# Optimization experiments

Hardware: AMD Instinct MI355X
Metric: run time of the kernel (lower is better)

Reference implementation:

```python
import jax, jax.numpy as jnp
import numpy as np

LAMBDA_DEPTHG = 0.3
STEGO_TEMPERATURE = 0.1
KNN_K = 7
DEPTH_SIGMA = 0.5
EPS = 1e-8


def _l2norm(x):
    return x / jnp.sqrt(jnp.sum(x * x, axis=-1, keepdims=True) + EPS)


def _stego_loss(codes, feats, temperature, knn_k):
    # Pairwise cosine similarity of DINO features -> KNN graph (includes self).
    f = _l2norm(feats)                                  # (B,N,Df)
    sim_f = jnp.einsum('bnd,bmd->bnm', f, f)            # (B,N,N)
    _, knn_idx = jax.lax.top_k(sim_f, knn_k)            # (B,N,k) int32
    # Temperature-scaled InfoNCE over code similarities; KNN entries are positives.
    c = _l2norm(codes)                                  # (B,N,Dc)
    logits = jnp.einsum('bnd,bmd->bnm', c, c) / temperature  # (B,N,N)
    logp = jax.nn.log_softmax(logits, axis=-1)          # (B,N,N)
    pos_logp = jnp.take_along_axis(logp, knn_idx, axis=-1)   # (B,N,k)
    return -jnp.mean(pos_logp)


def _depth_guided_correlation_loss(codes, depth, sigma_d):
    # Gaussian depth affinity: pixels at similar depth should have similar codes.
    dd = depth[:, :, None] - depth[:, None, :]          # (B,N,N)
    w = jnp.exp(-(dd * dd) / (2.0 * sigma_d * sigma_d)) # (B,N,N)
    c = _l2norm(codes)
    s = jnp.einsum('bnd,bmd->bnm', c, c)                # (B,N,N) cosine corr
    return jnp.mean(w * (1.0 - s))


def setup_inputs() -> dict:
    key = jax.random.key(0)
    k1, k2, k3 = jax.random.split(key, 3)
    B, N = 2, 4096
    semantic_codes = jax.random.normal(k1, (B, N, 90), dtype=jnp.float32)
    dino_features = jax.random.normal(k2, (B, N, 384), dtype=jnp.float32)
    depth = jax.random.uniform(k3, (B, N), dtype=jnp.float32)
    return {"semantic_codes": semantic_codes, "dino_features": dino_features, "depth": depth}


def reference(semantic_codes, dino_features, depth):
    l_stego = _stego_loss(semantic_codes, dino_features, STEGO_TEMPERATURE, KNN_K)
    l_depthg = _depth_guided_correlation_loss(semantic_codes, depth, DEPTH_SIGMA)
    total = l_stego + LAMBDA_DEPTHG * l_depthg
    return (l_stego, l_depthg, total)
```

## Files before the change

### kernel.cpp

```cpp
#include <hip/hip_runtime.h>
#include <math.h>

#define NPTS 4096

typedef __attribute__((ext_vector_type(8))) short bf16x8;
typedef __attribute__((ext_vector_type(16))) float f32x16;
typedef long fp8x8;

#define KEEP(x) asm volatile("" : "+v"(x))

__device__ __forceinline__ f32x16 zero16() {
  f32x16 z;
#pragma unroll
  for (int i = 0; i < 16; ++i) z[i] = 0.f;
  return z;
}

__device__ __forceinline__ unsigned packkey(float x, int m) {
  unsigned u = __float_as_uint(x);
  unsigned key = u ^ ((unsigned)((int)u >> 31) | 0x80000000u);
  return (key & 0xFFFFF000u) | (unsigned)m;
}

__device__ __forceinline__ void cas7(unsigned v, unsigned* s) {
#pragma unroll
  for (int t = 0; t < 7; ++t) {
    const unsigned hi = s[t] >= v ? s[t] : v;
    const unsigned lo = s[t] >= v ? v : s[t];
    s[t] = hi;
    v = lo;
  }
}

#define KSENT 0u

__device__ __forceinline__ unsigned bf16pack(float a, float b) {
  unsigned ua = __float_as_uint(a); ua = (ua + 0x7FFFu + ((ua >> 16) & 1u)) >> 16;
  unsigned ub = __float_as_uint(b); ub = (ub + 0x7FFFu + ((ub >> 16) & 1u)) >> 16;
  return ua | (ub << 16);
}

__global__ __launch_bounds__(64) void norm_all(const float* __restrict__ feats,
                                               const float* __restrict__ codes,
                                               unsigned char* __restrict__ Fsw8,
                                               unsigned short* __restrict__ Csw,
                                               float* __restrict__ invc) {
  const int row = blockIdx.x;
  const int lane = threadIdx.x;
  const int b = row >> 12, mt = (row >> 5) & 127, rl = row & 31;

  const float* f = feats + (size_t)row * 384;
  float v[8];
  float ss = 0.f;
  if (lane < 48) {
    float4 p0 = *(const float4*)(f + lane * 8);
    float4 p1 = *(const float4*)(f + lane * 8 + 4);
    v[0] = p0.x; v[1] = p0.y; v[2] = p0.z; v[3] = p0.w;
    v[4] = p1.x; v[5] = p1.y; v[6] = p1.z; v[7] = p1.w;
#pragma unroll
    for (int e = 0; e < 8; ++e) ss = fmaf(v[e], v[e], ss);
  }
#pragma unroll
  for (int m = 1; m <= 32; m <<= 1) ss += __shfl_xor(ss, m, 64);
  const float s8 = rsqrtf(ss + 1e-8f) * 8.0f;
  if (lane < 48) {
    int w0 = __builtin_amdgcn_cvt_pk_fp8_f32(v[0] * s8, v[1] * s8, 0, 0);
    w0 = __builtin_amdgcn_cvt_pk_fp8_f32(v[2] * s8, v[3] * s8, w0, 1);
    int w1 = __builtin_amdgcn_cvt_pk_fp8_f32(v[4] * s8, v[5] * s8, 0, 0);
    w1 = __builtin_amdgcn_cvt_pk_fp8_f32(v[6] * s8, v[7] * s8, w1, 1);
    const int kc = lane >> 1, hs = lane & 1;
    uint2 o = make_uint2((unsigned)w0, (unsigned)w1);
    *(uint2*)(Fsw8 + (((size_t)(b * 128 + mt) * 24 + kc) << 9) + (hs * 32 + rl) * 8) = o;
  }

  const float* c = codes + (size_t)row * 90;
  float cv[8];
#pragma unroll
  for (int e = 0; e < 8; ++e) cv[e] = 0.f;
  if (lane < 11) {
    float4 p0 = *(const float4*)(c + lane * 8);
    float4 p1 = *(const float4*)(c + lane * 8 + 4);
    cv[0] = p0.x; cv[1] = p0.y; cv[2] = p0.z; cv[3] = p0.w;
    cv[4] = p1.x; cv[5] = p1.y; cv[6] = p1.z; cv[7] = p1.w;
  } else if (lane == 11) {
    cv[0] = c[88]; cv[1] = c[89];
  }
  float cs = 0.f;
#pragma unroll
  for (int e = 0; e < 8; ++e) cs = fmaf(cv[e], cv[e], cs);
#pragma unroll
  for (int m = 1; m <= 32; m <<= 1) cs += __shfl_xor(cs, m, 64);
  const float cinv = rsqrtf(cs + 1e-8f);
  if (lane < 12) {
    uint4 o;
    o.x = bf16pack(cv[0] * cinv, cv[1] * cinv);
    o.y = bf16pack(cv[2] * cinv, cv[3] * cinv);
    o.z = bf16pack(cv[4] * cinv, cv[5] * cinv);
    o.w = bf16pack(cv[6] * cinv, cv[7] * cinv);
    const int kc = lane >> 1, hs = lane & 1;
    *(uint4*)(Csw + (((size_t)(b * 128 + mt) * 6 + kc) << 9) + (hs * 32 + rl) * 8) = o;
  }
  if (lane == 0) invc[row] = cinv;
}

__global__ __launch_bounds__(1024) void knn_mfma(const unsigned char* __restrict__ Fsw8,
                                                 unsigned* __restrict__ cand) {
  __shared__ unsigned long long qfrag[2 * 24 * 64];
  __shared__ unsigned ckey[16][64][7];
  const int g = blockIdx.x;
  const int b = g & 1;
  const int h = (g >> 1) & 1;
  const int qp = g >> 2;
  const int q0 = qp * 64;
  const int tid = threadIdx.x;
  const int w = tid >> 6;
  const int lane = tid & 63;
  const int lo = lane & 31, hi4 = (lane >> 5) * 4;
  const unsigned char* Fb = Fsw8 + (size_t)b * 128 * 24 * 512;

  {
    const unsigned long long* src =
        (const unsigned long long*)(Fb + ((size_t)(qp * 2) * 24) * 512);
#pragma unroll
    for (int k = 0; k < 3; ++k) qfrag[tid + k * 1024] = src[tid + k * 1024];
  }
  __syncthreads();

  unsigned s7a[7], s7b[7];
#pragma unroll
  for (int t = 0; t < 7; ++t) { s7a[t] = KSENT; s7b[t] = KSENT; }

  const int t0 = h * 64 + w * 4;
  const unsigned char* ab = Fb + ((size_t)t0 * 24) * 512 + lane * 8;

  fp8x8 a0[12], a1[12], bq[12];
#pragma unroll
  for (int t = 0; t < 12; ++t) a0[t] = *(const fp8x8*)(ab + t * 512);

  for (int mt = 0; mt < 4; ++mt) {
    const unsigned char* art = ab + (size_t)mt * 24 * 512;
#pragma unroll
    for (int t = 0; t < 12; ++t) a1[t] = *(const fp8x8*)(art + (12 + t) * 512);
    f32x16 acc0 = zero16(), acc1 = zero16();
#pragma unroll
    for (int t = 0; t < 12; ++t) bq[t] = (fp8x8)qfrag[t * 64 + lane];
#pragma unroll
    for (int t = 0; t < 12; ++t)
      acc0 = __builtin_amdgcn_mfma_f32_32x32x16_fp8_fp8(a0[t], bq[t], acc0, 0, 0, 0);
#pragma unroll
    for (int t = 0; t < 12; ++t) bq[t] = (fp8x8)qfrag[1536 + t * 64 + lane];
#pragma unroll
    for (int t = 0; t < 12; ++t)
      acc1 = __builtin_amdgcn_mfma_f32_32x32x16_fp8_fp8(a0[t], bq[t], acc1, 0, 0, 0);
#pragma unroll
    for (int t = 0; t < 12; ++t) KEEP(a1[t]);
    if (mt + 1 < 4) {
      const unsigned char* arn = ab + (size_t)(mt + 1) * 24 * 512;
#pragma unroll
      for (int t = 0; t < 12; ++t) a0[t] = *(const fp8x8*)(arn + t * 512);
    }
#pragma unroll
    for (int t = 0; t < 12; ++t) bq[t] = (fp8x8)qfrag[(12 + t) * 64 + lane];
#pragma unroll
    for (int t = 0; t < 12; ++t)
      acc0 = __builtin_amdgcn_mfma_f32_32x32x16_fp8_fp8(a1[t], bq[t], acc0, 0, 0, 0);
#pragma unroll
    for (int t = 0; t < 12; ++t) bq[t] = (fp8x8)qfrag[1536 + (12 + t) * 64 + lane];
#pragma unroll
    for (int t = 0; t < 12; ++t)
      acc1 = __builtin_amdgcn_mfma_f32_32x32x16_fp8_fp8(a1[t], bq[t], acc1, 0, 0, 0);
    const int mb = (t0 + mt) * 32 + hi4;
#pragma unroll
    for (int r = 0; r < 16; ++r) {
      const int m = mb + (r & 3) + 8 * (r >> 2);
      cas7(packkey(acc0[r], m), s7a);
      cas7(packkey(acc1[r], m), s7b);
    }
  }

#pragma unroll
  for (int t = 0; t < 7; ++t) {
    const unsigned ova = (unsigned)__shfl_xor((int)s7a[t], 32, 64);
    const unsigned ovb = (unsigned)__shfl_xor((int)s7b[t], 32, 64);
    cas7(ova, s7a);
    cas7(ovb, s7b);
  }
  if (lane < 32) {
#pragma unroll
    for (int t = 0; t < 7; ++t) {
      ckey[w][lo][t] = s7a[t];
      ckey[w][32 + lo][t] = s7b[t];
    }
  }
  __syncthreads();

  if (tid < 64) {
    unsigned fs[7];
#pragma unroll
    for (int t = 0; t < 7; ++t) fs[t] = KSENT;
    for (int w2 = 0; w2 < 16; ++w2)
#pragma unroll
      for (int t = 0; t < 7; ++t) cas7(ckey[w2][tid][t], fs);
    unsigned* o = cand + ((size_t)((h * 2 + b) * NPTS) + q0 + tid) * 7;
#pragma unroll
    for (int t = 0; t < 7; ++t) o[t] = fs[t];
  }
}

__global__ __launch_bounds__(1024) void lse_depth(const unsigned short* __restrict__ Csw,
                                                  const float* __restrict__ depth,
                                                  float* __restrict__ lse_out,
                                                  float* __restrict__ dpart) {
  __shared__ float lsep[16][32];
  __shared__ float depp[16];
  const int g = blockIdx.x;
  const int b = g & 1;
  const int qt = g >> 1;
  const int q0 = qt * 32;
  const int tid = threadIdx.x;
  const int w = tid >> 6;
  const int lane = tid & 63;
  const int lo = lane & 31, hi4 = (lane >> 5) * 4;
  const unsigned short* Cb = Csw + (size_t)b * 128 * 6 * 512;
  const float* db = depth + b * NPTS;

  bf16x8 bfr[6];
  {
    const unsigned short* qb = Cb + ((size_t)qt * 6) * 512 + lane * 8;
#pragma unroll
    for (int t = 0; t < 6; ++t) bfr[t] = *(const bf16x8*)(qb + t * 512);
#pragma unroll
    for (int t = 0; t < 6; ++t) KEEP(bfr[t]);
  }
  const float dq = db[q0 + lo];
  float slse = 0.f, sdep = 0.f;

  const int t0 = w * 8;
  const unsigned short* ab = Cb + ((size_t)t0 * 6) * 512 + lane * 8;

  bf16x8 a0[6], a1[6];
#pragma unroll
  for (int t = 0; t < 6; ++t) a0[t] = *(const bf16x8*)(ab + t * 512);
#pragma unroll
  for (int t = 0; t < 6; ++t) KEEP(a0[t]);

#define PROC3(A, GT)                                                           \
  {                                                                            \
    f32x16 acc = zero16();                                                     \
    _Pragma("unroll")                                                          \
    for (int t = 0; t < 6; ++t)                                                \
      acc = __builtin_amdgcn_mfma_f32_32x32x16_bf16(A[t], bfr[t], acc, 0, 0, 0); \
    float dvv[16];                                                             \
    _Pragma("unroll")                                                          \
    for (int k = 0; k < 4; ++k) {                                              \
      float4 dv = *(const float4*)(db + (GT) * 32 + hi4 + 8 * k);              \
      dvv[k * 4 + 0] = dv.x; dvv[k * 4 + 1] = dv.y;                            \
      dvv[k * 4 + 2] = dv.z; dvv[k * 4 + 3] = dv.w;                            \
    }                                                                          \
    _Pragma("unroll")                                                          \
    for (int r = 0; r < 16; ++r) {                                             \
      const float s = acc[r];                                                  \
      const float dd = dq - dvv[r];                                            \
      sdep += __expf(-2.f * dd * dd) * (1.f - s);                              \
      slse += __expf(fmaf(s, 10.f, -10.f));                                    \
    }                                                                          \
  }

  for (int mt = 0; mt < 8; mt += 2) {
    {
      const unsigned short* ar = ab + (size_t)(mt + 1) * 6 * 512;
#pragma unroll
      for (int t = 0; t < 6; ++t) a1[t] = *(const bf16x8*)(ar + t * 512);
    }
    PROC3(a0, t0 + mt)
#pragma unroll
    for (int t = 0; t < 6; ++t) KEEP(a1[t]);
    if (mt + 2 < 8) {
      const unsigned short* ar = ab + (size_t)(mt + 2) * 6 * 512;
#pragma unroll
      for (int t = 0; t < 6; ++t) a0[t] = *(const bf16x8*)(ar + t * 512);
    }
    PROC3(a1, t0 + mt + 1)
    if (mt + 2 < 8) {
#pragma unroll
      for (int t = 0; t < 6; ++t) KEEP(a0[t]);
    }
  }
#undef PROC3

  slse += __shfl_xor(slse, 32, 64);
  if (lane < 32) lsep[w][lo] = slse;
#pragma unroll
  for (int m = 1; m <= 32; m <<= 1) sdep += __shfl_xor(sdep, m, 64);
  if (lane == 0) depp[w] = sdep;
  __syncthreads();
  if (tid < 32) {
    float tot = 0.f;
#pragma unroll
    for (int w2 = 0; w2 < 16; ++w2) tot += lsep[w2][tid];
    lse_out[(size_t)(b * NPTS) + q0 + tid] = 10.f + __logf(tot);
  }
  if (tid == 32) {
    float d = 0.f;
#pragma unroll
    for (int w2 = 0; w2 < 16; ++w2) d += depp[w2];
    dpart[g] = d;
  }
}

__global__ __launch_bounds__(64) void gather_pos(const float* __restrict__ codes,
                                                 const float* __restrict__ invc,
                                                 const unsigned* __restrict__ cand,
                                                 float* __restrict__ gpart) {
  const int n = blockIdx.x;
  const int b = n >> 12, q = n & 4095;
  const int lane = threadIdx.x;

  unsigned s[7];
#pragma unroll
  for (int t = 0; t < 7; ++t) s[t] = KSENT;
  const unsigned* c0 = cand + ((size_t)(b * NPTS) + q) * 7;
  const unsigned* c1 = cand + ((size_t)((2 + b) * NPTS) + q) * 7;
#pragma unroll
  for (int t = 0; t < 7; ++t) cas7(c0[t], s);
#pragma unroll
  for (int t = 0; t < 7; ++t) cas7(c1[t], s);
  bool has = false;
#pragma unroll
  for (int t = 0; t < 7; ++t) has = has || ((s[t] & 4095u) == (unsigned)q);
  if (!has) s[6] = (unsigned)q;

  const float* cn = codes + (size_t)n * 90;
  float2 a = make_float2(0.f, 0.f);
  if (lane < 45) a = *(const float2*)(cn + lane * 2);
  const float inva = invc[n];
  float ssum = 0.f;
#pragma unroll
  for (int k = 0; k < 7; ++k) {
    const int m = (int)(s[k] & 4095u);
    const float* cm = codes + ((size_t)(b << 12) + m) * 90;
    float2 bb = make_float2(0.f, 0.f);
    if (lane < 45) bb = *(const float2*)(cm + lane * 2);
    float p = fmaf(a.x, bb.x, a.y * bb.y);
#pragma unroll
    for (int w = 1; w <= 32; w <<= 1) p += __shfl_xor(p, w, 64);
    ssum += p * inva * invc[(b << 12) + m];
  }
  if (lane == 0) gpart[n] = ssum;
}

__global__ __launch_bounds__(256) void finalize(const float* __restrict__ lse_out,
                                                const float* __restrict__ gpart,
                                                const float* __restrict__ dpart,
                                                float* __restrict__ out) {
  const int tid = threadIdx.x;
  float s1 = 0.f, s2 = 0.f;
  for (int n = tid; n < 2 * NPTS; n += 256) {
    s1 += lse_out[n];
    s2 += gpart[n];
  }
  float s3 = dpart[tid];
  __shared__ float r1[256], r2[256], r3[256];
  r1[tid] = s1; r2[tid] = s2; r3[tid] = s3;
  __syncthreads();
  for (int s = 128; s > 0; s >>= 1) {
    if (tid < s) { r1[tid] += r1[tid + s]; r2[tid] += r2[tid + s]; r3[tid] += r3[tid + s]; }
    __syncthreads();
  }
  if (tid == 0) {
    const float l_st = (7.f * r1[0] - 10.f * r2[0]) / 57344.f;
    const float l_dp = r3[0] / 33554432.f;
    out[0] = l_st;
    out[1] = l_dp;
    out[2] = l_st + 0.3f * l_dp;
  }
}

extern "C" void kernel_launch(void* const* d_in, const int* in_sizes, int n_in,
                              void* d_out, int out_size, void* d_ws, size_t ws_size,
                              hipStream_t stream) {
  (void)in_sizes; (void)n_in; (void)out_size; (void)ws_size;
  const float* codes = (const float*)d_in[0];
  const float* feats = (const float*)d_in[1];
  const float* depth = (const float*)d_in[2];
  float* out = (float*)d_out;

  char* ws = (char*)d_ws;
  float*    invc      = (float*)ws;
  unsigned* cand      = (unsigned*)(ws + 32768);
  unsigned char*  Fsw8 = (unsigned char*)(ws + 491520);
  unsigned short* Csw  = (unsigned short*)(ws + 3637248);
  float*    lse_out   = (float*)(ws + 5210112);
  float*    dpart     = (float*)(ws + 5242880);
  float*    gpart     = (float*)(ws + 5243904);

  norm_all<<<2 * NPTS, 64, 0, stream>>>(feats, codes, Fsw8, Csw, invc);
  knn_mfma<<<256, 1024, 0, stream>>>(Fsw8, cand);
  lse_depth<<<256, 1024, 0, stream>>>(Csw, depth, lse_out, dpart);
  gather_pos<<<2 * NPTS, 64, 0, stream>>>(codes, invc, cand, gpart);
  finalize<<<1, 256, 0, stream>>>(lse_out, gpart, dpart, out);
}
```

Baseline: 84.78 us.

## Replace pairwise depth loss with truncated Taylor moment expansion

Removes the per-pair Gaussian depth weight and correlation work from the N×N LSE kernel. exp(-2(dn-dm)^2) is factored as u_n u_m exp(4 dn dm), and exp(4 dn dm) is expanded as a 21-term Taylor series, so the depth loss becomes a sum of squared per-batch moment vectors. A new small kernel computes those moments and finalize combines them. This cuts the exp and FMA work in the hot MFMA loop, but the depth loss becomes a truncated-series approximation that relies on depth lying in [0,1]. It also adds one serial-ish kernel launch and a heavier finalize.

```diff
diff --git a/kernel.cpp b/kernel.cpp
--- a/kernel.cpp
+++ b/kernel.cpp
@@ -101,6 +101,36 @@
     *(uint4*)(Csw + (((size_t)(b * 128 + mt) * 6 + kc) << 9) + (hs * 32 + rl) * 8) = o;
   }
   if (lane == 0) invc[row] = cinv;
+}
+
+__global__ __launch_bounds__(128) void depth_moments(const float* __restrict__ codes,
+                                                     const float* __restrict__ invc,
+                                                     const float* __restrict__ depth,
+                                                     float* __restrict__ Gp) {
+  const int b = blockIdx.x & 1;
+  const int rc = blockIdx.x >> 1;
+  const int t = threadIdx.x;
+  float acc[21];
+#pragma unroll
+  for (int k = 0; k < 21; ++k) acc[k] = 0.f;
+  const int n0 = b * NPTS + rc * 128;
+  for (int i = 0; i < 128; ++i) {
+    const int n = n0 + i;
+    const float dn = depth[n];
+    const float u = __expf(-2.f * dn * dn);
+    float cd = 1.f;
+    if (t < 90) cd = codes[(size_t)n * 90 + t] * invc[n];
+    if (t < 91) {
+      float wk = u;
+#pragma unroll
+      for (int k = 0; k < 21; ++k) { acc[k] = fmaf(wk, cd, acc[k]); wk *= dn; }
+    }
+  }
+  if (t < 91) {
+#pragma unroll
+    for (int k = 0; k < 21; ++k)
+      Gp[((size_t)blockIdx.x * 21 + k) * 91 + t] = acc[k];
+  }
 }
 
 __global__ __launch_bounds__(1024) void knn_mfma(const unsigned char* __restrict__ Fsw8,
@@ -207,12 +237,9 @@
   }
 }
 
-__global__ __launch_bounds__(1024) void lse_depth(const unsigned short* __restrict__ Csw,
-                                                  const float* __restrict__ depth,
-                                                  float* __restrict__ lse_out,
-                                                  float* __restrict__ dpart) {
+__global__ __launch_bounds__(1024) void lse_only(const unsigned short* __restrict__ Csw,
+                                                 float* __restrict__ lse_out) {
   __shared__ float lsep[16][32];
-  __shared__ float depp[16];
   const int g = blockIdx.x;
   const int b = g & 1;
   const int qt = g >> 1;
@@ -220,9 +247,8 @@
   const int tid = threadIdx.x;
   const int w = tid >> 6;
   const int lane = tid & 63;
-  const int lo = lane & 31, hi4 = (lane >> 5) * 4;
+  const int lo = lane & 31;
   const unsigned short* Cb = Csw + (size_t)b * 128 * 6 * 512;
-  const float* db = depth + b * NPTS;
 
   bf16x8 bfr[6];
   {
@@ -232,8 +258,7 @@
 #pragma unroll
     for (int t = 0; t < 6; ++t) KEEP(bfr[t]);
   }
-  const float dq = db[q0 + lo];
-  float slse = 0.f, sdep = 0.f;
+  float slse = 0.f;
 
   const int t0 = w * 8;
   const unsigned short* ab = Cb + ((size_t)t0 * 6) * 512 + lane * 8;
@@ -244,26 +269,15 @@
 #pragma unroll
   for (int t = 0; t < 6; ++t) KEEP(a0[t]);
 
-#define PROC3(A, GT)                                                           \
+#define PROC3(A)                                                               \
   {                                                                            \
     f32x16 acc = zero16();                                                     \
     _Pragma("unroll")                                                          \
     for (int t = 0; t < 6; ++t)                                                \
       acc = __builtin_amdgcn_mfma_f32_32x32x16_bf16(A[t], bfr[t], acc, 0, 0, 0); \
-    float dvv[16];                                                             \
     _Pragma("unroll")                                                          \
-    for (int k = 0; k < 4; ++k) {                                              \
-      float4 dv = *(const float4*)(db + (GT) * 32 + hi4 + 8 * k);              \
-      dvv[k * 4 + 0] = dv.x; dvv[k * 4 + 1] = dv.y;                            \
-      dvv[k * 4 + 2] = dv.z; dvv[k * 4 + 3] = dv.w;                            \
-    }                                                                          \
-    _Pragma("unroll")                                                          \
-    for (int r = 0; r < 16; ++r) {                                             \
-      const float s = acc[r];                                                  \
-      const float dd = dq - dvv[r];                                            \
-      sdep += __expf(-2.f * dd * dd) * (1.f - s);                              \
-      slse += __expf(fmaf(s, 10.f, -10.f));                                    \
-    }                                                                          \
+    for (int r = 0; r < 16; ++r)                                               \
+      slse += __expf(fmaf(acc[r], 10.f, -10.f));                               \
   }
 
   for (int mt = 0; mt < 8; mt += 2) {
@@ -272,7 +286,7 @@
 #pragma unroll
       for (int t = 0; t < 6; ++t) a1[t] = *(const bf16x8*)(ar + t * 512);
     }
-    PROC3(a0, t0 + mt)
+    PROC3(a0)
 #pragma unroll
     for (int t = 0; t < 6; ++t) KEEP(a1[t]);
     if (mt + 2 < 8) {
@@ -280,7 +294,7 @@
 #pragma unroll
       for (int t = 0; t < 6; ++t) a0[t] = *(const bf16x8*)(ar + t * 512);
     }
-    PROC3(a1, t0 + mt + 1)
+    PROC3(a1)
     if (mt + 2 < 8) {
 #pragma unroll
       for (int t = 0; t < 6; ++t) KEEP(a0[t]);
@@ -290,21 +304,12 @@
 
   slse += __shfl_xor(slse, 32, 64);
   if (lane < 32) lsep[w][lo] = slse;
-#pragma unroll
-  for (int m = 1; m <= 32; m <<= 1) sdep += __shfl_xor(sdep, m, 64);
-  if (lane == 0) depp[w] = sdep;
   __syncthreads();
   if (tid < 32) {
     float tot = 0.f;
 #pragma unroll
     for (int w2 = 0; w2 < 16; ++w2) tot += lsep[w2][tid];
     lse_out[(size_t)(b * NPTS) + q0 + tid] = 10.f + __logf(tot);
-  }
-  if (tid == 32) {
-    float d = 0.f;
-#pragma unroll
-    for (int w2 = 0; w2 < 16; ++w2) d += depp[w2];
-    dpart[g] = d;
   }
 }
 
@@ -351,7 +356,7 @@
 
 __global__ __launch_bounds__(256) void finalize(const float* __restrict__ lse_out,
                                                 const float* __restrict__ gpart,
-                                                const float* __restrict__ dpart,
+                                                const float* __restrict__ Gp,
                                                 float* __restrict__ out) {
   const int tid = threadIdx.x;
   float s1 = 0.f, s2 = 0.f;
@@ -359,7 +364,18 @@
     s1 += lse_out[n];
     s2 += gpart[n];
   }
-  float s3 = dpart[tid];
+  float s3 = 0.f;
+  for (int e = tid; e < 2 * 21 * 91; e += 256) {
+    const int b = e / (21 * 91);
+    const int rem = e % (21 * 91);
+    const int k = rem / 91, d = rem % 91;
+    float G = 0.f;
+    for (int rc = 0; rc < 32; ++rc)
+      G += Gp[((size_t)(rc * 2 + b) * 21 + k) * 91 + d];
+    float ck = 1.f;
+    for (int i = 1; i <= k; ++i) ck *= 4.f / (float)i;
+    s3 += (d == 90 ? ck : -ck) * G * G;
+  }
   __shared__ float r1[256], r2[256], r3[256];
   r1[tid] = s1; r2[tid] = s2; r3[tid] = s3;
   __syncthreads();
@@ -391,12 +407,13 @@
   unsigned char*  Fsw8 = (unsigned char*)(ws + 491520);
   unsigned short* Csw  = (unsigned short*)(ws + 3637248);
   float*    lse_out   = (float*)(ws + 5210112);
-  float*    dpart     = (float*)(ws + 5242880);
-  float*    gpart     = (float*)(ws + 5243904);
+  float*    gpart     = (float*)(ws + 5242880);
+  float*    Gp        = (float*)(ws + 5275648);
 
   norm_all<<<2 * NPTS, 64, 0, stream>>>(feats, codes, Fsw8, Csw, invc);
+  depth_moments<<<64, 128, 0, stream>>>(codes, invc, depth, Gp);
   knn_mfma<<<256, 1024, 0, stream>>>(Fsw8, cand);
-  lse_depth<<<256, 1024, 0, stream>>>(Csw, depth, lse_out, dpart);
+  lse_only<<<256, 1024, 0, stream>>>(Csw, lse_out);
   gather_pos<<<2 * NPTS, 64, 0, stream>>>(codes, invc, cand, gpart);
-  finalize<<<1, 256, 0, stream>>>(lse_out, gpart, dpart, out);
-}
+  finalize<<<1, 256, 0, stream>>>(lse_out, gpart, Gp, out);
+}
```

New measurement: 140.1 us. +65.3%, slower.
